# Kernel optimization log

Measured on AMD Instinct MI355X. Metric: run time of the kernel, lower is better.

## Reference

```python
import jax, jax.numpy as jnp
import numpy as np

N_IN, N_OUT, N_HID = 4, 3, 64
N = N_OUT + N_HID  # 67 neurons (outputs first, matching neuron_key2idx ordering)
H, W = 1024, 1024


def setup_inputs() -> dict:
    key = jax.random.key(0)
    ks = jax.random.split(key, 6)
    inputs = jax.random.normal(ks[0], (H, W, N_IN), jnp.float32)
    # sparse NEAT connectivity encoded as masked dense matrices
    m_in = (jax.random.uniform(ks[1], (N_IN, N)) < 0.5).astype(jnp.float32)
    m_rec = (jax.random.uniform(ks[2], (N, N)) < 0.25).astype(jnp.float32)
    W_in = jax.random.normal(ks[3], (N_IN, N), jnp.float32) * m_in
    W_rec = jax.random.normal(ks[4], (N, N), jnp.float32) * 0.3 * m_rec
    bias = jax.random.normal(ks[5], (N,), jnp.float32) * 0.1
    response = jnp.ones((N,), jnp.float32)
    # neurons with no incoming connections output exactly 0 (original code path)
    has_in = ((m_in.sum(0) + m_rec.sum(0)) > 0).astype(jnp.float32)
    return {"inputs": inputs, "W_in": W_in, "W_rec": W_rec, "bias": bias,
            "response": response, "has_in": has_in, "n_passes": 2}


def reference(inputs, W_in, W_rec, bias, response, has_in, n_passes):
    lead = inputs.shape[:-1]
    x = inputs.reshape(-1, inputs.shape[-1])  # [B, N_IN]
    activs = jnp.zeros((x.shape[0], bias.shape[0]), x.dtype)  # [B, N]
    for _ in range(n_passes):  # small fixed recurrent pass count
        # sum-aggregation of weighted incoming edges from inputs and prev activs
        agg = x @ W_in + activs @ W_rec  # [B, N]
        activs = has_in * jnp.tanh(bias + response * agg)
    out = activs[:, :N_OUT]
    return out.reshape(lead + (N_OUT,))
```

## Files before the change

kernel.cpp:

```cpp
#include <hip/hip_runtime.h>

#define NN   67
#define NOUT 3
#define NIN  4
#define PKW  16
#define PK_FLOATS (NN * PKW)
#define PK_BYTES  (PK_FLOATS * 4)
#define C2   2.885390081777927f

#if __has_builtin(__builtin_amdgcn_exp2f)
  #define EXP2F __builtin_amdgcn_exp2f
#else
  #define EXP2F exp2f
#endif
#if __has_builtin(__builtin_amdgcn_rcpf)
  #define RCPF __builtin_amdgcn_rcpf
#else
  #define RCPF(x) (1.0f/(x))
#endif

__device__ __forceinline__ float tanh_sc(float arg) {
    float e = EXP2F(arg);
    float r = RCPF(e + 1.0f);
    return __builtin_fmaf(-2.0f, r, 1.0f);
}

__global__ void pack_kernel(const float* __restrict__ Win,
                            const float* __restrict__ Wrec,
                            const float* __restrict__ bias,
                            const float* __restrict__ resp,
                            const float* __restrict__ hasin,
                            float* __restrict__ pk)
{
    int j = threadIdx.x;
    if (j < NN) {
        float h = hasin[j];
        float* p = pk + j * PKW;
        p[0] = Win[0*NN + j]; p[1] = Win[1*NN + j];
        p[2] = Win[2*NN + j]; p[3] = Win[3*NN + j];
        p[4] = resp[j] * h * C2;
        p[5] = bias[j] * h * C2;
        p[6] = Wrec[j*NN + 0]; p[7] = Wrec[j*NN + 1]; p[8] = Wrec[j*NN + 2];
        p[9]=p[10]=p[11]=p[12]=p[13]=p[14]=p[15] = 0.f;
    }
}

template<int P>
__global__ __launch_bounds__(256)
void rnn_fused(const float* __restrict__ inputs,
               const float* __restrict__ pk,
               const float* __restrict__ Wrec,
               const int*   __restrict__ np_ptr,
               float*       __restrict__ out,
               int total)
{
    __shared__ __align__(16) float spk[PK_FLOATS];
    {
        float4*       d = reinterpret_cast<float4*>(spk);
        const float4* s = reinterpret_cast<const float4*>(pk);
        #pragma unroll
        for (int t = 0; t < 2; ++t) {
            int i = threadIdx.x + t * 256;
            if (i < PK_FLOATS / 4) d[i] = s[i];
        }
    }
    __syncthreads();

    const int np   = np_ptr[0];
    const int base = blockIdx.x * (256 * P) + threadIdx.x;

    int    pix[P];
    float4 x[P];
#pragma unroll
    for (int p = 0; p < P; ++p) {
        pix[p] = base + p * 256;
        int idx = pix[p] < total ? pix[p] : total - 1;
        x[p] = reinterpret_cast<const float4*>(inputs)[idx];
    }

    float res[P][NOUT];

    if (np == 2) {
        float acc[P][NOUT];
#pragma unroll
        for (int p = 0; p < P; ++p)
#pragma unroll
            for (int c = 0; c < NOUT; ++c) {
                const float* q = &spk[c * PKW];
                float a = x[p].x * q[0];
                a = __builtin_fmaf(x[p].y, q[1], a);
                a = __builtin_fmaf(x[p].z, q[2], a);
                a = __builtin_fmaf(x[p].w, q[3], a);
                acc[p][c] = a;
            }
#pragma unroll
        for (int j = 0; j < NN; ++j) {
            const float* q = &spk[j * PKW];
            const float4 qa = *reinterpret_cast<const float4*>(q);
            const float4 qb = *reinterpret_cast<const float4*>(q + 4);
            const float  wr2 = q[8];
#pragma unroll
            for (int p = 0; p < P; ++p) {
                float agg = x[p].x * qa.x;
                agg = __builtin_fmaf(x[p].y, qa.y, agg);
                agg = __builtin_fmaf(x[p].z, qa.z, agg);
                agg = __builtin_fmaf(x[p].w, qa.w, agg);
                float a = tanh_sc(__builtin_fmaf(qb.x, agg, qb.y));
                acc[p][0] = __builtin_fmaf(a, qb.z, acc[p][0]);
                acc[p][1] = __builtin_fmaf(a, qb.w, acc[p][1]);
                acc[p][2] = __builtin_fmaf(a, wr2,  acc[p][2]);
            }
        }
#pragma unroll
        for (int p = 0; p < P; ++p)
#pragma unroll
            for (int c = 0; c < NOUT; ++c) {
                const float* q = &spk[c * PKW];
                res[p][c] = tanh_sc(__builtin_fmaf(q[4], acc[p][c], q[5]));
            }
    } else if (np <= 0) {
#pragma unroll
        for (int p = 0; p < P; ++p)
#pragma unroll
            for (int c = 0; c < NOUT; ++c) res[p][c] = 0.f;
    } else if (np == 1) {
#pragma unroll
        for (int p = 0; p < P; ++p)
#pragma unroll
            for (int c = 0; c < NOUT; ++c) {
                const float* q = &spk[c * PKW];
                float agg = x[p].x * q[0];
                agg = __builtin_fmaf(x[p].y, q[1], agg);
                agg = __builtin_fmaf(x[p].z, q[2], agg);
                agg = __builtin_fmaf(x[p].w, q[3], agg);
                res[p][c] = tanh_sc(__builtin_fmaf(q[4], agg, q[5]));
            }
    } else {
#pragma unroll
        for (int p = 0; p < P; ++p) {
            float act[NN];
            #pragma unroll 1
            for (int j = 0; j < NN; ++j) {
                const float* q = &spk[j * PKW];
                float agg = x[p].x * q[0];
                agg = __builtin_fmaf(x[p].y, q[1], agg);
                agg = __builtin_fmaf(x[p].z, q[2], agg);
                agg = __builtin_fmaf(x[p].w, q[3], agg);
                act[j] = tanh_sc(__builtin_fmaf(q[4], agg, q[5]));
            }
            #pragma unroll 1
            for (int t = 1; t < np - 1; ++t) {
                float na[NN];
                #pragma unroll 1
                for (int j = 0; j < NN; ++j) {
                    const float* q = &spk[j * PKW];
                    float agg = x[p].x * q[0];
                    agg = __builtin_fmaf(x[p].y, q[1], agg);
                    agg = __builtin_fmaf(x[p].z, q[2], agg);
                    agg = __builtin_fmaf(x[p].w, q[3], agg);
                    #pragma unroll 1
                    for (int k = 0; k < NN; ++k)
                        agg = __builtin_fmaf(act[k], Wrec[k*NN + j], agg);
                    na[j] = tanh_sc(__builtin_fmaf(q[4], agg, q[5]));
                }
                #pragma unroll 1
                for (int j = 0; j < NN; ++j) act[j] = na[j];
            }
            #pragma unroll
            for (int c = 0; c < NOUT; ++c) {
                const float* q = &spk[c * PKW];
                float agg = x[p].x * q[0];
                agg = __builtin_fmaf(x[p].y, q[1], agg);
                agg = __builtin_fmaf(x[p].z, q[2], agg);
                agg = __builtin_fmaf(x[p].w, q[3], agg);
                #pragma unroll 1
                for (int k = 0; k < NN; ++k)
                    agg = __builtin_fmaf(act[k], Wrec[k*NN + c], agg);
                res[p][c] = tanh_sc(__builtin_fmaf(q[4], agg, q[5]));
            }
        }
    }

#pragma unroll
    for (int p = 0; p < P; ++p)
        if (pix[p] < total) {
            out[pix[p]*NOUT + 0] = res[p][0];
            out[pix[p]*NOUT + 1] = res[p][1];
            out[pix[p]*NOUT + 2] = res[p][2];
        }
}

__global__ __launch_bounds__(256)
void rnn_general(const float* __restrict__ inputs,
                 const float* __restrict__ Win,
                 const float* __restrict__ Wrec,
                 const float* __restrict__ bias,
                 const float* __restrict__ resp,
                 const float* __restrict__ hasin,
                 const int*   __restrict__ np_ptr,
                 float*       __restrict__ out, int total)
{
    int pix = blockIdx.x * blockDim.x + threadIdx.x;
    if (pix >= total) return;
    const int np = np_ptr[0];
    const float4 x = reinterpret_cast<const float4*>(inputs)[pix];
    float act[NN];
    #pragma unroll 1
    for (int j = 0; j < NN; ++j) act[j] = 0.f;
    #pragma unroll 1
    for (int t = 0; t < np; ++t) {
        float na[NN];
        #pragma unroll 1
        for (int j = 0; j < NN; ++j) {
            float agg = x.x * Win[0*NN+j];
            agg = __builtin_fmaf(x.y, Win[1*NN+j], agg);
            agg = __builtin_fmaf(x.z, Win[2*NN+j], agg);
            agg = __builtin_fmaf(x.w, Win[3*NN+j], agg);
            #pragma unroll 1
            for (int k = 0; k < NN; ++k)
                agg = __builtin_fmaf(act[k], Wrec[k*NN + j], agg);
            na[j] = hasin[j] * tanh_sc(C2 * __builtin_fmaf(resp[j], agg, bias[j]));
        }
        #pragma unroll 1
        for (int j = 0; j < NN; ++j) act[j] = na[j];
    }
    out[pix*NOUT+0] = act[0]; out[pix*NOUT+1] = act[1]; out[pix*NOUT+2] = act[2];
}

extern "C" void kernel_launch(void* const* d_in, const int* in_sizes, int n_in,
                              void* d_out, int out_size, void* d_ws, size_t ws_size,
                              hipStream_t stream) {
    const float* inputs = (const float*)d_in[0];
    const float* Win    = (const float*)d_in[1];
    const float* Wrec   = (const float*)d_in[2];
    const float* bias   = (const float*)d_in[3];
    const float* resp   = (const float*)d_in[4];
    const float* hasin  = (const float*)d_in[5];
    const int*   np     = (const int*)d_in[6];
    float*       out    = (float*)d_out;

    const int total = in_sizes[0] / NIN;

    if (ws_size >= (size_t)PK_BYTES) {
        float* pkbuf = (float*)d_ws;
        pack_kernel<<<1, 128, 0, stream>>>(Win, Wrec, bias, resp, hasin, pkbuf);
        constexpr int P = 2;
        const int block = 256;
        const int grid  = (total + block * P - 1) / (block * P);
        rnn_fused<P><<<grid, block, 0, stream>>>(inputs, pkbuf, Wrec, np, out, total);
    } else {
        const int block = 256;
        const int grid  = (total + block - 1) / block;
        rnn_general<<<grid, block, 0, stream>>>(inputs, Win, Wrec, bias, resp,
                                                hasin, np, out, total);
    }
}
```

Baseline: 105.6 us.

## Pack pixel pairs into float2 vectors for packed FMA and raise pixels per thread

The np==2 path now transposes pairs of pixels into two-wide float vectors so the input dot products and recurrent accumulations can map to packed FMA instructions on CDNA. exp and rcp are issued through inline asm as v_exp_f32/v_rcp_f32, and pixels per thread go from 2 to 4, which halves the grid and amortises the shared-memory weight loads over more pixels. The aim is to cut VALU instruction count. In exchange, register pressure rises and inline asm may block some scheduling optimisations.

```diff
diff --git a/kernel.cpp b/kernel.cpp
--- a/kernel.cpp
+++ b/kernel.cpp
@@ -8,20 +8,22 @@
 #define PK_BYTES  (PK_FLOATS * 4)
 #define C2   2.885390081777927f
 
-#if __has_builtin(__builtin_amdgcn_exp2f)
-  #define EXP2F __builtin_amdgcn_exp2f
-#else
-  #define EXP2F exp2f
-#endif
-#if __has_builtin(__builtin_amdgcn_rcpf)
-  #define RCPF __builtin_amdgcn_rcpf
-#else
-  #define RCPF(x) (1.0f/(x))
-#endif
+typedef float v2f __attribute__((ext_vector_type(2)));
+
+__device__ __forceinline__ v2f vfma(v2f a, v2f b, v2f c) {
+    return __builtin_elementwise_fma(a, b, c);
+}
+
+__device__ __forceinline__ float fexp2(float x) {
+    float r; asm("v_exp_f32 %0, %1" : "=v"(r) : "v"(x)); return r;
+}
+__device__ __forceinline__ float frcp(float x) {
+    float r; asm("v_rcp_f32 %0, %1" : "=v"(r) : "v"(x)); return r;
+}
 
 __device__ __forceinline__ float tanh_sc(float arg) {
-    float e = EXP2F(arg);
-    float r = RCPF(e + 1.0f);
+    float e = fexp2(arg);
+    float r = frcp(e + 1.0f);
     return __builtin_fmaf(-2.0f, r, 1.0f);
 }
 
@@ -54,12 +56,15 @@
                float*       __restrict__ out,
                int total)
 {
+    static_assert(P % 2 == 0, "P must be even");
+    constexpr int NC = P / 2;
+
     __shared__ __align__(16) float spk[PK_FLOATS];
     {
         float4*       d = reinterpret_cast<float4*>(spk);
         const float4* s = reinterpret_cast<const float4*>(pk);
         #pragma unroll
-        for (int t = 0; t < 2; ++t) {
+        for (int t = 0; t < (PK_FLOATS/4 + 255) / 256; ++t) {
             int i = threadIdx.x + t * 256;
             if (i < PK_FLOATS / 4) d[i] = s[i];
         }
@@ -81,59 +86,81 @@
     float res[P][NOUT];
 
     if (np == 2) {
-        float acc[P][NOUT];
-#pragma unroll
-        for (int p = 0; p < P; ++p)
-#pragma unroll
-            for (int c = 0; c < NOUT; ++c) {
-                const float* q = &spk[c * PKW];
-                float a = x[p].x * q[0];
-                a = __builtin_fmaf(x[p].y, q[1], a);
-                a = __builtin_fmaf(x[p].z, q[2], a);
-                a = __builtin_fmaf(x[p].w, q[3], a);
-                acc[p][c] = a;
-            }
+        v2f xf[NIN][NC];
+#pragma unroll
+        for (int c = 0; c < NC; ++c) {
+            xf[0][c] = v2f{x[2*c].x, x[2*c+1].x};
+            xf[1][c] = v2f{x[2*c].y, x[2*c+1].y};
+            xf[2][c] = v2f{x[2*c].z, x[2*c+1].z};
+            xf[3][c] = v2f{x[2*c].w, x[2*c+1].w};
+        }
+
+        v2f acc[NOUT][NC];
+#pragma unroll
+        for (int o = 0; o < NOUT; ++o) {
+            const float* q = &spk[o * PKW];
+            const v2f w0 = {q[0], q[0]}, w1 = {q[1], q[1]},
+                      w2 = {q[2], q[2]}, w3 = {q[3], q[3]};
+#pragma unroll
+            for (int c = 0; c < NC; ++c) {
+                v2f a = xf[0][c] * w0;
+                a = vfma(xf[1][c], w1, a);
+                a = vfma(xf[2][c], w2, a);
+                a = vfma(xf[3][c], w3, a);
+                acc[o][c] = a;
+            }
+        }
+
 #pragma unroll
         for (int j = 0; j < NN; ++j) {
             const float* q = &spk[j * PKW];
             const float4 qa = *reinterpret_cast<const float4*>(q);
             const float4 qb = *reinterpret_cast<const float4*>(q + 4);
-            const float  wr2 = q[8];
-#pragma unroll
-            for (int p = 0; p < P; ++p) {
-                float agg = x[p].x * qa.x;
-                agg = __builtin_fmaf(x[p].y, qa.y, agg);
-                agg = __builtin_fmaf(x[p].z, qa.z, agg);
-                agg = __builtin_fmaf(x[p].w, qa.w, agg);
-                float a = tanh_sc(__builtin_fmaf(qb.x, agg, qb.y));
-                acc[p][0] = __builtin_fmaf(a, qb.z, acc[p][0]);
-                acc[p][1] = __builtin_fmaf(a, qb.w, acc[p][1]);
-                acc[p][2] = __builtin_fmaf(a, wr2,  acc[p][2]);
-            }
-        }
+            const float  wr2s = q[8];
+            const v2f w0  = {qa.x, qa.x}, w1 = {qa.y, qa.y},
+                      w2  = {qa.z, qa.z}, w3 = {qa.w, qa.w};
+            const v2f r2  = {qb.x, qb.x}, b2 = {qb.y, qb.y};
+            const v2f wr0 = {qb.z, qb.z}, wr1 = {qb.w, qb.w}, wr2 = {wr2s, wr2s};
+#pragma unroll
+            for (int c = 0; c < NC; ++c) {
+                v2f agg = xf[0][c] * w0;
+                agg = vfma(xf[1][c], w1, agg);
+                agg = vfma(xf[2][c], w2, agg);
+                agg = vfma(xf[3][c], w3, agg);
+                v2f arg = vfma(r2, agg, b2);
+                v2f a = v2f{tanh_sc(arg.x), tanh_sc(arg.y)};
+                acc[0][c] = vfma(a, wr0, acc[0][c]);
+                acc[1][c] = vfma(a, wr1, acc[1][c]);
+                acc[2][c] = vfma(a, wr2, acc[2][c]);
+            }
+        }
+
+#pragma unroll
+        for (int o = 0; o < NOUT; ++o) {
+            const float* q = &spk[o * PKW];
+            const float r2s = q[4], b2s = q[5];
+#pragma unroll
+            for (int c = 0; c < NC; ++c) {
+                res[2*c  ][o] = tanh_sc(__builtin_fmaf(r2s, acc[o][c].x, b2s));
+                res[2*c+1][o] = tanh_sc(__builtin_fmaf(r2s, acc[o][c].y, b2s));
+            }
+        }
+    } else if (np <= 0) {
 #pragma unroll
         for (int p = 0; p < P; ++p)
 #pragma unroll
-            for (int c = 0; c < NOUT; ++c) {
-                const float* q = &spk[c * PKW];
-                res[p][c] = tanh_sc(__builtin_fmaf(q[4], acc[p][c], q[5]));
-            }
-    } else if (np <= 0) {
+            for (int o = 0; o < NOUT; ++o) res[p][o] = 0.f;
+    } else if (np == 1) {
 #pragma unroll
         for (int p = 0; p < P; ++p)
 #pragma unroll
-            for (int c = 0; c < NOUT; ++c) res[p][c] = 0.f;
-    } else if (np == 1) {
-#pragma unroll
-        for (int p = 0; p < P; ++p)
-#pragma unroll
-            for (int c = 0; c < NOUT; ++c) {
-                const float* q = &spk[c * PKW];
+            for (int o = 0; o < NOUT; ++o) {
+                const float* q = &spk[o * PKW];
                 float agg = x[p].x * q[0];
                 agg = __builtin_fmaf(x[p].y, q[1], agg);
                 agg = __builtin_fmaf(x[p].z, q[2], agg);
                 agg = __builtin_fmaf(x[p].w, q[3], agg);
-                res[p][c] = tanh_sc(__builtin_fmaf(q[4], agg, q[5]));
+                res[p][o] = tanh_sc(__builtin_fmaf(q[4], agg, q[5]));
             }
     } else {
 #pragma unroll
@@ -167,16 +194,16 @@
                 for (int j = 0; j < NN; ++j) act[j] = na[j];
             }
             #pragma unroll
-            for (int c = 0; c < NOUT; ++c) {
-                const float* q = &spk[c * PKW];
+            for (int o = 0; o < NOUT; ++o) {
+                const float* q = &spk[o * PKW];
                 float agg = x[p].x * q[0];
                 agg = __builtin_fmaf(x[p].y, q[1], agg);
                 agg = __builtin_fmaf(x[p].z, q[2], agg);
                 agg = __builtin_fmaf(x[p].w, q[3], agg);
                 #pragma unroll 1
                 for (int k = 0; k < NN; ++k)
-                    agg = __builtin_fmaf(act[k], Wrec[k*NN + c], agg);
-                res[p][c] = tanh_sc(__builtin_fmaf(q[4], agg, q[5]));
+                    agg = __builtin_fmaf(act[k], Wrec[k*NN + o], agg);
+                res[p][o] = tanh_sc(__builtin_fmaf(q[4], agg, q[5]));
             }
         }
     }
@@ -244,7 +271,7 @@
     if (ws_size >= (size_t)PK_BYTES) {
         float* pkbuf = (float*)d_ws;
         pack_kernel<<<1, 128, 0, stream>>>(Win, Wrec, bias, resp, hasin, pkbuf);
-        constexpr int P = 2;
+        constexpr int P = 4;
         const int block = 256;
         const int grid  = (total + block * P - 1) / (block * P);
         rnn_fused<P><<<grid, block, 0, stream>>>(inputs, pkbuf, Wrec, np, out, total);
```

After: 103.6 us. Within noise of the previous version (-1.9%).
